# Kernel tuning notes

Hardware: AMD Instinct MI355X
Metric: run time of the kernel (lower is better)

## Reference

```python
import jax, jax.numpy as jnp
import numpy as np

K = 7          # involution kernel size
P = 3          # padding = (K-1)//2
GC = 16        # group_channels in involution
EPS = 1e-5


def bn(x, g, b):
    # training-mode BatchNorm2d forward: per-channel batch stats over (B,H,W)
    m = jnp.mean(x, axis=(0, 2, 3), keepdims=True)
    v = jnp.var(x, axis=(0, 2, 3), keepdims=True)
    return (x - m) * jax.lax.rsqrt(v + EPS) * g[None, :, None, None] + b[None, :, None, None]


def conv1x1(x, w):
    # x: [B,C,H,W], w: [O,C] -> [B,O,H,W]
    return jnp.einsum('bchw,oc->bohw', x, w)


def unfold7(x):
    # torch F.unfold(kernel=7, pad=3, stride=1) -> [B, C, K*K, H, W] (C slowest, matching torch layout)
    B, C, H, W = x.shape
    xp = jnp.pad(x, ((0, 0), (0, 0), (P, P), (P, P)))
    return jnp.stack([xp[:, :, i:i + H, j:j + W] for i in range(K) for j in range(K)], axis=2)


def involution(x, wr, gr, br, ws):
    # kernel generation: 1x1 reduce -> BN -> ReLU -> 1x1 span to G*K*K per-pixel kernels
    B, C, H, W = x.shape
    G = C // GC
    t = jax.nn.relu(bn(conv1x1(x, wr), gr, br))          # [B, C//4, H, W]
    w = conv1x1(t, ws).reshape(B, G, 1, K * K, H, W)     # per-pixel kernels
    p = unfold7(x).reshape(B, G, GC, K * K, H, W)        # unfolded patches
    return jnp.sum(w * p, axis=3).reshape(B, C, H, W)    # multiply-accumulate over K*K


def setup_inputs() -> dict:
    key = jax.random.key(0)
    ks = jax.random.split(key, 14)
    Cin, Cout, mid = 256, 256, 64
    red = mid // 4                 # reduction_ratio = 4
    G = mid // GC                  # groups = 4
    s = lambda *sh: 1.0 / np.sqrt(np.prod(sh[1:]) if len(sh) > 1 else sh[0])
    return {
        'x':  jax.random.normal(ks[0], (8, Cin, 56, 56), jnp.float32),
        'w1': jax.random.normal(ks[1], (mid, Cin), jnp.float32) * s(mid, Cin),
        'g1': jnp.ones((mid,), jnp.float32),
        'b1': jnp.zeros((mid,), jnp.float32),
        'wr': jax.random.normal(ks[2], (red, mid), jnp.float32) * s(red, mid),
        'gr': jnp.ones((red,), jnp.float32),
        'br': jnp.zeros((red,), jnp.float32),
        'ws': jax.random.normal(ks[3], (K * K * G, red), jnp.float32) * s(K * K * G, red),
        'g2': jnp.ones((mid,), jnp.float32),
        'b2': jnp.zeros((mid,), jnp.float32),
        'w3': jax.random.normal(ks[4], (Cout, mid), jnp.float32) * s(Cout, mid),
        'g3': jnp.ones((Cout,), jnp.float32),
        'b3': jnp.zeros((Cout,), jnp.float32),
    }


def reference(x, w1, g1, b1, wr, gr, br, ws, g2, b2, w3, g3, b3):
    out = jax.nn.relu(bn(conv1x1(x, w1), g1, b1))        # conv1 1x1 + BN + ReLU
    out = jax.nn.relu(bn(involution(out, wr, gr, br, ws), g2, b2))  # involution + BN + ReLU
    out = bn(conv1x1(out, w3), g3, b3)                   # conv3 1x1 + BN
    return jax.nn.relu(out + x)                          # residual add + ReLU
```

## Files before the change

kernel.cpp:

```cpp
#include <hip/hip_runtime.h>

#define HW 3136
#define NPIX 25088
#define NBLK 392

#define OFF_Y1   0u
#define OFF_TR   1605632u
#define OFF_WT   2007040u
#define OFF_OUT2 6924288u
#define OFF_Y3   8529920u
#define OFF_ST   14952448u
#define ACC1 0
#define ACCR 128
#define ACC2 160
#define ACC3 288
#define FIN1 800
#define FINR 928
#define FIN2 960
#define FIN3 1088

__device__ __forceinline__ float wave_sum(float v) {
    #pragma unroll
    for (int off = 32; off > 0; off >>= 1) v += __shfl_xor(v, off, 64);
    return v;
}

__device__ __forceinline__ void gl_lds16(const float* g, float* l) {
    __builtin_amdgcn_global_load_lds(
        (const __attribute__((address_space(1))) unsigned int*)g,
        (__attribute__((address_space(3))) unsigned int*)l, 16, 0, 0);
}

__global__ __launch_bounds__(256) void k_wt(const float* __restrict__ w1,
        const float* __restrict__ w3, float* __restrict__ w1t, float* __restrict__ w3t) {
    int i = blockIdx.x * 256 + threadIdx.x;
    if (i < 16384) {
        int oc = i >> 8, ic = i & 255;
        w1t[ic * 64 + oc] = w1[i];
    } else {
        int j = i - 16384;
        int oc = j >> 6, ic = j & 63;
        w3t[ic * 256 + oc] = w3[j];
    }
}

__global__ __launch_bounds__(256) void k_conv1(const float* __restrict__ x,
        const float* __restrict__ w1t, float* __restrict__ y1, float* __restrict__ st) {
    __shared__ float xs[2][64][64];
    __shared__ float ws[2][64][64];
    int t = threadIdx.x, pb = blockIdx.x;
    int b = pb / 49, hw0 = (pb % 49) * 64;
    int tx = t & 15, ty = t >> 4;
    int wv = t >> 6, ln = t & 63;

    #define STAGE(cc, buf)                                                        \
        _Pragma("unroll")                                                         \
        for (int i = 0; i < 4; i++) {                                             \
            int s = i * 4 + wv;                                                   \
            const float* gx = x + (size_t)((b * 256) + (cc) * 64 + s * 4 + (ln >> 4)) * HW \
                              + hw0 + (ln & 15) * 4;                              \
            gl_lds16(gx, &xs[buf][s * 4][0]);                                     \
            const float* gw = w1t + ((cc) * 64 + s * 4) * 64 + ln * 4;            \
            gl_lds16(gw, &ws[buf][s * 4][0]);                                     \
        }

    STAGE(0, 0);
    __syncthreads();
    float acc[4][4];
    #pragma unroll
    for (int i = 0; i < 4; i++)
        #pragma unroll
        for (int j = 0; j < 4; j++) acc[i][j] = 0.f;
    #pragma unroll 1
    for (int cc = 0; cc < 4; cc++) {
        int cur = cc & 1;
        if (cc < 3) STAGE(cc + 1, cur ^ 1);
        #pragma unroll 8
        for (int c = 0; c < 64; c++) {
            float4 xv = *(const float4*)&xs[cur][c][tx * 4];
            float4 wv4 = *(const float4*)&ws[cur][c][ty * 4];
            float xa[4] = {xv.x, xv.y, xv.z, xv.w};
            float wa[4] = {wv4.x, wv4.y, wv4.z, wv4.w};
            #pragma unroll
            for (int i = 0; i < 4; i++)
                #pragma unroll
                for (int j = 0; j < 4; j++) acc[i][j] = fmaf(wa[i], xa[j], acc[i][j]);
        }
        __syncthreads();
    }
    #undef STAGE
    #pragma unroll
    for (int i = 0; i < 4; i++) {
        int oc = ty * 4 + i;
        float4 o = make_float4(acc[i][0], acc[i][1], acc[i][2], acc[i][3]);
        *(float4*)&y1[((b * 64) + oc) * HW + hw0 + tx * 4] = o;
        float s = o.x + o.y + o.z + o.w;
        float q = o.x * o.x + o.y * o.y + o.z * o.z + o.w * o.w;
        #pragma unroll
        for (int off = 1; off <= 8; off <<= 1) {
            s += __shfl_xor(s, off, 64);
            q += __shfl_xor(q, off, 64);
        }
        if (tx == 0) {
            atomicAdd(&st[ACC1 + oc], s);
            atomicAdd(&st[ACC1 + 64 + oc], q);
        }
    }
}

__global__ void k_fin(const float* __restrict__ acc, float* __restrict__ fin,
                      const float* __restrict__ gamma, const float* __restrict__ beta, int C) {
    int c = threadIdx.x;
    if (c < C) {
        float mean = acc[c] * (1.0f / (float)NPIX);
        float var  = acc[C + c] * (1.0f / (float)NPIX) - mean * mean;
        float rstd = rsqrtf(var + 1e-5f);
        float a = gamma[c] * rstd;
        fin[c] = a;
        fin[C + c] = beta[c] - mean * a;
    }
}

__global__ __launch_bounds__(256, 4) void k_bn1_convr(const float* __restrict__ y1,
        const float* __restrict__ wr, float* __restrict__ tr, float* __restrict__ st) {
    __shared__ float ys[64][64];
    __shared__ float wsh[16][64];
    int t = threadIdx.x, pb = blockIdx.x;
    int b = pb / 49, hw0 = (pb % 49) * 64;
    int tx = t & 15, ty = t >> 4;
    #pragma unroll
    for (int i = 0; i < 16; i++) {
        int e = i * 256 + t, c = e >> 6, p = e & 63;
        float v = y1[((b * 64) + c) * HW + hw0 + p];
        ys[c][p] = fmaxf(st[FIN1 + c] * v + st[FIN1 + 64 + c], 0.f);
    }
    #pragma unroll
    for (int i = 0; i < 4; i++) {
        int e = i * 256 + t;
        wsh[e >> 6][e & 63] = wr[e];
    }
    __syncthreads();
    float a0 = 0.f, a1 = 0.f, a2 = 0.f, a3 = 0.f;
    #pragma unroll 8
    for (int c = 0; c < 64; c++) {
        float4 yv = *(const float4*)&ys[c][tx * 4];
        float wv = wsh[ty][c];
        a0 = fmaf(wv, yv.x, a0); a1 = fmaf(wv, yv.y, a1);
        a2 = fmaf(wv, yv.z, a2); a3 = fmaf(wv, yv.w, a3);
    }
    *(float4*)&tr[((b * 16) + ty) * HW + hw0 + tx * 4] = make_float4(a0, a1, a2, a3);
    float s = a0 + a1 + a2 + a3;
    float q = a0 * a0 + a1 * a1 + a2 * a2 + a3 * a3;
    #pragma unroll
    for (int off = 1; off <= 8; off <<= 1) {
        s += __shfl_xor(s, off, 64);
        q += __shfl_xor(q, off, 64);
    }
    if (tx == 0) {
        atomicAdd(&st[ACCR + ty], s);
        atomicAdd(&st[ACCR + 16 + ty], q);
    }
}

__global__ __launch_bounds__(256) void k_invol(const float* __restrict__ y1,
        const float* __restrict__ tr, const float* __restrict__ wsp,
        float* __restrict__ out2, float* __restrict__ st) {
    __shared__ float ts[16][256];
    __shared__ float sw[49][16];
    __shared__ float ps[8][10][64];
    __shared__ float red[4][16];
    int t = threadIdx.x, bidx = blockIdx.x;
    int h = bidx & 1, r2 = bidx >> 1;
    int ht = r2 % 14;
    int bg = r2 / 14;
    int g = bg & 3, b = bg >> 2;
    int h0 = ht * 4;
    int c0 = h * 8;
    #pragma unroll
    for (int i = 0; i < 16; i++) {
        int e = i * 256 + t, c = e >> 8, p = e & 255;
        if (p < 224) {
            float v = tr[((b * 16) + c) * HW + h0 * 56 + p];
            ts[c][p] = fmaxf(st[FINR + c] * v + st[FINR + 16 + c], 0.f);
        }
    }
    for (int e = t; e < 784; e += 256) sw[e >> 4][e & 15] = wsp[g * 784 + e];
    for (int i = 0; i < 20; i++) {
        int e = i * 256 + t;
        int c = e / 640, rem = e - c * 640;
        int r = rem >> 6, wc = rem & 63;
        int gh = h0 + r - 3, gw = wc - 3;
        float v = 0.f;
        if (gh >= 0 && gh < 56 && gw >= 0 && gw < 56) {
            int ch = g * 16 + c0 + c;
            float raw = y1[((b * 64) + ch) * HW + gh * 56 + gw];
            v = fmaxf(st[FIN1 + ch] * raw + st[FIN1 + 64 + ch], 0.f);
        }
        ps[c][r][wc] = v;
    }
    __syncthreads();
    float accv[8];
    #pragma unroll
    for (int c = 0; c < 8; c++) accv[c] = 0.f;
    bool active = t < 224;
    if (active) {
        int lh = t / 56, lw = t % 56;
        float tsr[16];
        #pragma unroll
        for (int c = 0; c < 16; c++) tsr[c] = ts[c][t];
        float kr[49];
        #pragma unroll
        for (int k = 0; k < 49; k++) {
            const float4* swr = (const float4*)&sw[k][0];
            float4 u0 = swr[0], u1 = swr[1], u2 = swr[2], u3 = swr[3];
            float v = u0.x * tsr[0];
            v = fmaf(u0.y, tsr[1], v);  v = fmaf(u0.z, tsr[2], v);  v = fmaf(u0.w, tsr[3], v);
            v = fmaf(u1.x, tsr[4], v);  v = fmaf(u1.y, tsr[5], v);  v = fmaf(u1.z, tsr[6], v);
            v = fmaf(u1.w, tsr[7], v);  v = fmaf(u2.x, tsr[8], v);  v = fmaf(u2.y, tsr[9], v);
            v = fmaf(u2.z, tsr[10], v); v = fmaf(u2.w, tsr[11], v); v = fmaf(u3.x, tsr[12], v);
            v = fmaf(u3.y, tsr[13], v); v = fmaf(u3.z, tsr[14], v); v = fmaf(u3.w, tsr[15], v);
            kr[k] = v;
        }
        #pragma unroll
        for (int k = 0; k < 49; k++) {
            int ki = k / 7, kj = k % 7;
            float kv = kr[k];
            #pragma unroll
            for (int c = 0; c < 8; c++)
                accv[c] = fmaf(kv, ps[c][lh + ki][lw + kj], accv[c]);
        }
        int hw = h0 * 56 + t;
        #pragma unroll
        for (int c = 0; c < 8; c++)
            out2[((b * 64) + g * 16 + c0 + c) * HW + hw] = accv[c];
    }
    int wave = t >> 6, lane = t & 63;
    #pragma unroll
    for (int c = 0; c < 8; c++) {
        float v = active ? accv[c] : 0.f;
        float s  = wave_sum(v);
        float s2 = wave_sum(v * v);
        if (lane == 0) { red[wave][c] = s; red[wave][8 + c] = s2; }
    }
    __syncthreads();
    if (t < 16) {
        float s = red[0][t] + red[1][t] + red[2][t] + red[3][t];
        int c = t & 7, isq = t >> 3;
        atomicAdd(&st[ACC2 + isq * 64 + g * 16 + c0 + c], s);
    }
}

__global__ __launch_bounds__(256, 4) void k_bn2_conv3(const float* __restrict__ out2,
        const float* __restrict__ w3t, float* __restrict__ y3, float* __restrict__ st) {
    __shared__ float os[64][64];
    __shared__ float wst[64][64];
    int t = threadIdx.x, blk = blockIdx.x;
    int occ = blk & 3, pb = blk >> 2;
    int b = pb / 49, hw0 = (pb % 49) * 64;
    int tx = t & 15, ty = t >> 4;
    #pragma unroll
    for (int i = 0; i < 16; i++) {
        int e = i * 256 + t, c = e >> 6, p = e & 63;
        float v = out2[((b * 64) + c) * HW + hw0 + p];
        os[c][p] = fmaxf(st[FIN2 + c] * v + st[FIN2 + 64 + c], 0.f);
        wst[c][p] = w3t[c * 256 + occ * 64 + p];
    }
    __syncthreads();
    float acc[4][4];
    #pragma unroll
    for (int i = 0; i < 4; i++)
        #pragma unroll
        for (int j = 0; j < 4; j++) acc[i][j] = 0.f;
    #pragma unroll 8
    for (int c = 0; c < 64; c++) {
        float4 xv = *(const float4*)&os[c][tx * 4];
        float4 wv = *(const float4*)&wst[c][ty * 4];
        float xa[4] = {xv.x, xv.y, xv.z, xv.w};
        float wa[4] = {wv.x, wv.y, wv.z, wv.w};
        #pragma unroll
        for (int i = 0; i < 4; i++)
            #pragma unroll
            for (int j = 0; j < 4; j++) acc[i][j] = fmaf(wa[i], xa[j], acc[i][j]);
    }
    #pragma unroll
    for (int i = 0; i < 4; i++) {
        int oc = occ * 64 + ty * 4 + i;
        float4 o = make_float4(acc[i][0], acc[i][1], acc[i][2], acc[i][3]);
        *(float4*)&y3[((b * 256) + oc) * HW + hw0 + tx * 4] = o;
        float s = o.x + o.y + o.z + o.w;
        float q = o.x * o.x + o.y * o.y + o.z * o.z + o.w * o.w;
        #pragma unroll
        for (int off = 1; off <= 8; off <<= 1) {
            s += __shfl_xor(s, off, 64);
            q += __shfl_xor(q, off, 64);
        }
        if (tx == 0) {
            atomicAdd(&st[ACC3 + oc], s);
            atomicAdd(&st[ACC3 + 256 + oc], q);
        }
    }
}

__global__ __launch_bounds__(256) void k_final(const float* __restrict__ y3,
        const float* __restrict__ x, float* __restrict__ out, const float* __restrict__ st) {
    int idx = blockIdx.x * 256 + threadIdx.x;
    if (idx < 1605632) {
        int c = (idx / 784) & 255;
        float a = st[FIN3 + c], bb = st[FIN3 + 256 + c];
        float4 v  = ((const float4*)y3)[idx];
        float4 xv = ((const float4*)x)[idx];
        float4 o;
        o.x = fmaxf(a * v.x + bb + xv.x, 0.f);
        o.y = fmaxf(a * v.y + bb + xv.y, 0.f);
        o.z = fmaxf(a * v.z + bb + xv.z, 0.f);
        o.w = fmaxf(a * v.w + bb + xv.w, 0.f);
        ((float4*)out)[idx] = o;
    }
}

extern "C" void kernel_launch(void* const* d_in, const int* in_sizes, int n_in,
                              void* d_out, int out_size, void* d_ws, size_t ws_size,
                              hipStream_t stream) {
    const float* x   = (const float*)d_in[0];
    const float* w1  = (const float*)d_in[1];
    const float* g1  = (const float*)d_in[2];
    const float* b1  = (const float*)d_in[3];
    const float* wr  = (const float*)d_in[4];
    const float* gr  = (const float*)d_in[5];
    const float* br  = (const float*)d_in[6];
    const float* wsp = (const float*)d_in[7];
    const float* g2  = (const float*)d_in[8];
    const float* b2  = (const float*)d_in[9];
    const float* w3  = (const float*)d_in[10];
    const float* g3  = (const float*)d_in[11];
    const float* b3  = (const float*)d_in[12];
    float* out = (float*)d_out;
    float* w   = (float*)d_ws;
    float* y1   = w + OFF_Y1;
    float* tr   = w + OFF_TR;
    float* w1t  = w + OFF_WT;
    float* w3t  = w + OFF_WT + 16384;
    float* out2 = w + OFF_OUT2;
    float* y3   = w + OFF_Y3;
    float* st   = w + OFF_ST;

    hipMemsetAsync(st, 0, 2048 * sizeof(float), stream);
    k_wt<<<128, 256, 0, stream>>>(w1, w3, w1t, w3t);
    k_conv1<<<NBLK, 256, 0, stream>>>(x, w1t, y1, st);
    k_fin<<<1, 64, 0, stream>>>(st + ACC1, st + FIN1, g1, b1, 64);
    k_bn1_convr<<<NBLK, 256, 0, stream>>>(y1, wr, tr, st);
    k_fin<<<1, 64, 0, stream>>>(st + ACCR, st + FINR, gr, br, 16);
    k_invol<<<896, 256, 0, stream>>>(y1, tr, wsp, out2, st);
    k_fin<<<1, 64, 0, stream>>>(st + ACC2, st + FIN2, g2, b2, 64);
    k_bn2_conv3<<<NBLK * 4, 256, 0, stream>>>(out2, w3t, y3, st);
    k_fin<<<1, 256, 0, stream>>>(st + ACC3, st + FIN3, g3, b3, 256);
    k_final<<<6272, 256, 0, stream>>>(y3, x, out, st);
}
```

Baseline: 275.1 us.

## Use bf16 MFMA for conv1 and conv3 with pixel-major transposed bf16 inputs

Replaces the fp32 FMA tiled GEMMs for conv1 and conv3 with bf16 MFMA 16x16x32 instructions. A new pass transposes x into a pixel-major bf16 layout with an XOR-swizzled LDS-friendly addressing. The involution kernel now writes its output as pixel-major bf16, and conv3 runs one block per pixel tile covering all 256 output channels instead of four blocks. The aim is to cut ALU time and memory traffic, at the cost of an extra transpose pass over x and reduced precision from bf16 rounding of activations and weights.

Result: no change. 274.5 us (-0.2%).

```diff
diff --git a/kernel.cpp b/kernel.cpp
--- a/kernel.cpp
+++ b/kernel.cpp
@@ -4,12 +4,17 @@
 #define NPIX 25088
 #define NBLK 392
 
-#define OFF_Y1   0u
-#define OFF_TR   1605632u
-#define OFF_WT   2007040u
-#define OFF_OUT2 6924288u
-#define OFF_Y3   8529920u
-#define OFF_ST   14952448u
+typedef float f32x4 __attribute__((ext_vector_type(4)));
+typedef short short8 __attribute__((ext_vector_type(8)));
+
+#define OFF_Y1    0u
+#define OFF_TR    1605632u
+#define OFF_W1BF  2007040u
+#define OFF_W3BF  2015232u
+#define OFF_XT    2023424u
+#define OFF_OUT2T 5234688u
+#define OFF_Y3    6037504u
+#define OFF_ST    12460032u
 #define ACC1 0
 #define ACCR 128
 #define ACC2 160
@@ -24,84 +29,105 @@
     for (int off = 32; off > 0; off >>= 1) v += __shfl_xor(v, off, 64);
     return v;
 }
-
-__device__ __forceinline__ void gl_lds16(const float* g, float* l) {
+__device__ __forceinline__ unsigned short f2bf(float f) {
+    unsigned u = __float_as_uint(f);
+    u += 0x7FFFu + ((u >> 16) & 1u);
+    return (unsigned short)(u >> 16);
+}
+__device__ __forceinline__ float bf2f(unsigned h) {
+    return __uint_as_float(h << 16);
+}
+__device__ __forceinline__ void gl_lds16(const void* g, void* l) {
     __builtin_amdgcn_global_load_lds(
         (const __attribute__((address_space(1))) unsigned int*)g,
         (__attribute__((address_space(3))) unsigned int*)l, 16, 0, 0);
 }
 
-__global__ __launch_bounds__(256) void k_wt(const float* __restrict__ w1,
-        const float* __restrict__ w3, float* __restrict__ w1t, float* __restrict__ w3t) {
+__global__ __launch_bounds__(256) void k_prep(const float* __restrict__ w1,
+        const float* __restrict__ w3, unsigned short* __restrict__ w1bf,
+        unsigned short* __restrict__ w3bf) {
     int i = blockIdx.x * 256 + threadIdx.x;
-    if (i < 16384) {
-        int oc = i >> 8, ic = i & 255;
-        w1t[ic * 64 + oc] = w1[i];
-    } else {
-        int j = i - 16384;
-        int oc = j >> 6, ic = j & 63;
-        w3t[ic * 256 + oc] = w3[j];
-    }
-}
-
-__global__ __launch_bounds__(256) void k_conv1(const float* __restrict__ x,
-        const float* __restrict__ w1t, float* __restrict__ y1, float* __restrict__ st) {
-    __shared__ float xs[2][64][64];
-    __shared__ float ws[2][64][64];
+    if (i < 16384) w1bf[i] = f2bf(w1[i]);
+    else w3bf[i - 16384] = f2bf(w3[i - 16384]);
+}
+
+__global__ __launch_bounds__(256) void k_tx(const float* __restrict__ x,
+        unsigned short* __restrict__ xt) {
+    __shared__ float lt[64][65];
+    int t = threadIdx.x, bidx = blockIdx.x;
+    int ict = bidx & 3, r = bidx >> 2;
+    int pt = r % 49, b = r / 49;
+    int pix0 = pt * 64, ic0 = ict * 64;
+    #pragma unroll
+    for (int i = 0; i < 16; i++) {
+        int e = i * 256 + t, ic = e >> 6, p = e & 63;
+        lt[ic][p] = x[(size_t)((b * 256) + ic0 + ic) * HW + pix0 + p];
+    }
+    __syncthreads();
+    char* tb = (char*)xt + (size_t)(b * HW + pix0) * 512;
+    #pragma unroll
+    for (int i = 0; i < 2; i++) {
+        int c = i * 256 + t;
+        int p = c >> 3, q = c & 7;
+        uint4 o;
+        o.x = f2bf(lt[q * 8 + 0][p]) | ((unsigned)f2bf(lt[q * 8 + 1][p]) << 16);
+        o.y = f2bf(lt[q * 8 + 2][p]) | ((unsigned)f2bf(lt[q * 8 + 3][p]) << 16);
+        o.z = f2bf(lt[q * 8 + 4][p]) | ((unsigned)f2bf(lt[q * 8 + 5][p]) << 16);
+        o.w = f2bf(lt[q * 8 + 6][p]) | ((unsigned)f2bf(lt[q * 8 + 7][p]) << 16);
+        unsigned d = (unsigned)(p * 512 + (ic0 + q * 8) * 2) ^ (unsigned)((p & 7) << 4);
+        *(uint4*)(tb + d) = o;
+    }
+}
+
+__global__ __launch_bounds__(256, 4) void k_conv1(const unsigned short* __restrict__ xt,
+        const unsigned short* __restrict__ w1bf, float* __restrict__ y1,
+        float* __restrict__ st) {
+    __shared__ unsigned short xs[64 * 256];
     int t = threadIdx.x, pb = blockIdx.x;
     int b = pb / 49, hw0 = (pb % 49) * 64;
-    int tx = t & 15, ty = t >> 4;
-    int wv = t >> 6, ln = t & 63;
-
-    #define STAGE(cc, buf)                                                        \
-        _Pragma("unroll")                                                         \
-        for (int i = 0; i < 4; i++) {                                             \
-            int s = i * 4 + wv;                                                   \
-            const float* gx = x + (size_t)((b * 256) + (cc) * 64 + s * 4 + (ln >> 4)) * HW \
-                              + hw0 + (ln & 15) * 4;                              \
-            gl_lds16(gx, &xs[buf][s * 4][0]);                                     \
-            const float* gw = w1t + ((cc) * 64 + s * 4) * 64 + ln * 4;            \
-            gl_lds16(gw, &ws[buf][s * 4][0]);                                     \
-        }
-
-    STAGE(0, 0);
-    __syncthreads();
-    float acc[4][4];
-    #pragma unroll
-    for (int i = 0; i < 4; i++)
-        #pragma unroll
-        for (int j = 0; j < 4; j++) acc[i][j] = 0.f;
-    #pragma unroll 1
-    for (int cc = 0; cc < 4; cc++) {
-        int cur = cc & 1;
-        if (cc < 3) STAGE(cc + 1, cur ^ 1);
-        #pragma unroll 8
-        for (int c = 0; c < 64; c++) {
-            float4 xv = *(const float4*)&xs[cur][c][tx * 4];
-            float4 wv4 = *(const float4*)&ws[cur][c][ty * 4];
-            float xa[4] = {xv.x, xv.y, xv.z, xv.w};
-            float wa[4] = {wv4.x, wv4.y, wv4.z, wv4.w};
-            #pragma unroll
-            for (int i = 0; i < 4; i++)
-                #pragma unroll
-                for (int j = 0; j < 4; j++) acc[i][j] = fmaf(wa[i], xa[j], acc[i][j]);
-        }
-        __syncthreads();
-    }
-    #undef STAGE
-    #pragma unroll
-    for (int i = 0; i < 4; i++) {
-        int oc = ty * 4 + i;
-        float4 o = make_float4(acc[i][0], acc[i][1], acc[i][2], acc[i][3]);
-        *(float4*)&y1[((b * 64) + oc) * HW + hw0 + tx * 4] = o;
-        float s = o.x + o.y + o.z + o.w;
-        float q = o.x * o.x + o.y * o.y + o.z * o.z + o.w * o.w;
+    int lane = t & 63, wv = t >> 6;
+    int grp = lane >> 4, li = lane & 15;
+    int oc0 = wv * 16;
+    short8 a[8];
+    #pragma unroll
+    for (int s = 0; s < 8; s++)
+        a[s] = *(const short8*)(w1bf + (size_t)(oc0 + li) * 256 + s * 32 + grp * 8);
+    const char* src = (const char*)xt + (size_t)(b * HW + hw0) * 512;
+    char* dst = (char*)xs;
+    #pragma unroll
+    for (int i = 0; i < 8; i++)
+        gl_lds16(src + wv * 8192 + i * 1024 + lane * 16, dst + wv * 8192 + i * 1024);
+    __syncthreads();
+    f32x4 acc[4];
+    #pragma unroll
+    for (int n = 0; n < 4; n++) acc[n] = (f32x4){0.f, 0.f, 0.f, 0.f};
+    #pragma unroll
+    for (int s = 0; s < 8; s++) {
+        #pragma unroll
+        for (int n = 0; n < 4; n++) {
+            int row = n * 16 + li;
+            unsigned o = (unsigned)(row * 512 + s * 64 + grp * 16) ^ (unsigned)((row & 7) << 4);
+            short8 bf = *(const short8*)(dst + o);
+            acc[n] = __builtin_amdgcn_mfma_f32_16x16x32_bf16(a[s], bf, acc[n], 0, 0, 0);
+        }
+    }
+    #pragma unroll
+    for (int n = 0; n < 4; n++)
+        #pragma unroll
+        for (int r = 0; r < 4; r++)
+            y1[(size_t)(b * 64 + oc0 + grp * 4 + r) * HW + hw0 + n * 16 + li] = acc[n][r];
+    #pragma unroll
+    for (int r = 0; r < 4; r++) {
+        float s = acc[0][r] + acc[1][r] + acc[2][r] + acc[3][r];
+        float q = acc[0][r] * acc[0][r] + acc[1][r] * acc[1][r]
+                + acc[2][r] * acc[2][r] + acc[3][r] * acc[3][r];
         #pragma unroll
         for (int off = 1; off <= 8; off <<= 1) {
             s += __shfl_xor(s, off, 64);
             q += __shfl_xor(q, off, 64);
         }
-        if (tx == 0) {
+        if (li == 0) {
+            int oc = oc0 + grp * 4 + r;
             atomicAdd(&st[ACC1 + oc], s);
             atomicAdd(&st[ACC1 + 64 + oc], q);
         }
@@ -164,18 +190,18 @@
 
 __global__ __launch_bounds__(256) void k_invol(const float* __restrict__ y1,
         const float* __restrict__ tr, const float* __restrict__ wsp,
-        float* __restrict__ out2, float* __restrict__ st) {
+        unsigned short* __restrict__ out2t, float* __restrict__ st) {
     __shared__ float ts[16][256];
     __shared__ float sw[49][16];
     __shared__ float ps[8][10][64];
     __shared__ float red[4][16];
     int t = threadIdx.x, bidx = blockIdx.x;
-    int h = bidx & 1, r2 = bidx >> 1;
+    int hh = bidx & 1, r2 = bidx >> 1;
     int ht = r2 % 14;
     int bg = r2 / 14;
     int g = bg & 3, b = bg >> 2;
     int h0 = ht * 4;
-    int c0 = h * 8;
+    int c0 = hh * 8;
     #pragma unroll
     for (int i = 0; i < 16; i++) {
         int e = i * 256 + t, c = e >> 8, p = e & 255;
@@ -230,9 +256,12 @@
                 accv[c] = fmaf(kv, ps[c][lh + ki][lw + kj], accv[c]);
         }
         int hw = h0 * 56 + t;
-        #pragma unroll
-        for (int c = 0; c < 8; c++)
-            out2[((b * 64) + g * 16 + c0 + c) * HW + hw] = accv[c];
+        uint4 o;
+        o.x = f2bf(accv[0]) | ((unsigned)f2bf(accv[1]) << 16);
+        o.y = f2bf(accv[2]) | ((unsigned)f2bf(accv[3]) << 16);
+        o.z = f2bf(accv[4]) | ((unsigned)f2bf(accv[5]) << 16);
+        o.w = f2bf(accv[6]) | ((unsigned)f2bf(accv[7]) << 16);
+        *(uint4*)((char*)out2t + (size_t)(b * HW + hw) * 128 + (g * 16 + c0) * 2) = o;
     }
     int wave = t >> 6, lane = t & 63;
     #pragma unroll
@@ -250,53 +279,89 @@
     }
 }
 
-__global__ __launch_bounds__(256, 4) void k_bn2_conv3(const float* __restrict__ out2,
-        const float* __restrict__ w3t, float* __restrict__ y3, float* __restrict__ st) {
-    __shared__ float os[64][64];
-    __shared__ float wst[64][64];
-    int t = threadIdx.x, blk = blockIdx.x;
-    int occ = blk & 3, pb = blk >> 2;
+__global__ __launch_bounds__(256, 2) void k_bn2c3(const unsigned short* __restrict__ out2t,
+        const unsigned short* __restrict__ w3bf, float* __restrict__ y3,
+        float* __restrict__ st) {
+    __shared__ unsigned short bs[64 * 64];
+    __shared__ float sa[64], sb[64];
+    int t = threadIdx.x, pb = blockIdx.x;
     int b = pb / 49, hw0 = (pb % 49) * 64;
-    int tx = t & 15, ty = t >> 4;
-    #pragma unroll
-    for (int i = 0; i < 16; i++) {
-        int e = i * 256 + t, c = e >> 6, p = e & 63;
-        float v = out2[((b * 64) + c) * HW + hw0 + p];
-        os[c][p] = fmaxf(st[FIN2 + c] * v + st[FIN2 + 64 + c], 0.f);
-        wst[c][p] = w3t[c * 256 + occ * 64 + p];
-    }
-    __syncthreads();
-    float acc[4][4];
-    #pragma unroll
-    for (int i = 0; i < 4; i++)
-        #pragma unroll
-        for (int j = 0; j < 4; j++) acc[i][j] = 0.f;
-    #pragma unroll 8
-    for (int c = 0; c < 64; c++) {
-        float4 xv = *(const float4*)&os[c][tx * 4];
-        float4 wv = *(const float4*)&wst[c][ty * 4];
-        float xa[4] = {xv.x, xv.y, xv.z, xv.w};
-        float wa[4] = {wv.x, wv.y, wv.z, wv.w};
-        #pragma unroll
-        for (int i = 0; i < 4; i++)
+    int lane = t & 63, wv = t >> 6;
+    int grp = lane >> 4, li = lane & 15;
+    if (t < 64) sa[t] = st[FIN2 + t];
+    else if (t < 128) { int c = t - 64; sb[c] = st[FIN2 + 64 + c]; }
+    short8 a[8];
+    #pragma unroll
+    for (int m = 0; m < 4; m++)
+        #pragma unroll
+        for (int s = 0; s < 2; s++)
+            a[m * 2 + s] = *(const short8*)(w3bf
+                + (size_t)(wv * 64 + m * 16 + li) * 64 + s * 32 + grp * 8);
+    __syncthreads();
+    #pragma unroll
+    for (int i = 0; i < 2; i++) {
+        int c = i * 256 + t, p = c >> 3, q = c & 7;
+        uint4 v = *(const uint4*)((const char*)out2t + (size_t)(b * HW + hw0 + p) * 128 + q * 16);
+        float4 fa0 = *(const float4*)&sa[q * 8];
+        float4 fa1 = *(const float4*)&sa[q * 8 + 4];
+        float4 fb0 = *(const float4*)&sb[q * 8];
+        float4 fb1 = *(const float4*)&sb[q * 8 + 4];
+        float e0 = fmaxf(fa0.x * bf2f(v.x & 0xFFFFu) + fb0.x, 0.f);
+        float e1 = fmaxf(fa0.y * bf2f(v.x >> 16) + fb0.y, 0.f);
+        float e2 = fmaxf(fa0.z * bf2f(v.y & 0xFFFFu) + fb0.z, 0.f);
+        float e3 = fmaxf(fa0.w * bf2f(v.y >> 16) + fb0.w, 0.f);
+        float e4 = fmaxf(fa1.x * bf2f(v.z & 0xFFFFu) + fb1.x, 0.f);
+        float e5 = fmaxf(fa1.y * bf2f(v.z >> 16) + fb1.y, 0.f);
+        float e6 = fmaxf(fa1.z * bf2f(v.w & 0xFFFFu) + fb1.z, 0.f);
+        float e7 = fmaxf(fa1.w * bf2f(v.w >> 16) + fb1.w, 0.f);
+        uint4 o;
+        o.x = f2bf(e0) | ((unsigned)f2bf(e1) << 16);
+        o.y = f2bf(e2) | ((unsigned)f2bf(e3) << 16);
+        o.z = f2bf(e4) | ((unsigned)f2bf(e5) << 16);
+        o.w = f2bf(e6) | ((unsigned)f2bf(e7) << 16);
+        unsigned d = (unsigned)(p * 128 + q * 16) ^ (unsigned)((p & 7) << 4);
+        *(uint4*)((char*)bs + d) = o;
+    }
+    __syncthreads();
+    f32x4 acc[4][4];
+    #pragma unroll
+    for (int m = 0; m < 4; m++)
+        #pragma unroll
+        for (int n = 0; n < 4; n++) acc[m][n] = (f32x4){0.f, 0.f, 0.f, 0.f};
+    #pragma unroll
+    for (int s = 0; s < 2; s++)
+        #pragma unroll
+        for (int n = 0; n < 4; n++) {
+            int row = n * 16 + li;
+            unsigned o = (unsigned)(row * 128 + s * 64 + grp * 16) ^ (unsigned)((row & 7) << 4);
+            short8 bf = *(const short8*)((const char*)bs + o);
             #pragma unroll
-            for (int j = 0; j < 4; j++) acc[i][j] = fmaf(wa[i], xa[j], acc[i][j]);
-    }
-    #pragma unroll
-    for (int i = 0; i < 4; i++) {
-        int oc = occ * 64 + ty * 4 + i;
-        float4 o = make_float4(acc[i][0], acc[i][1], acc[i][2], acc[i][3]);
-        *(float4*)&y3[((b * 256) + oc) * HW + hw0 + tx * 4] = o;
-        float s = o.x + o.y + o.z + o.w;
-        float q = o.x * o.x + o.y * o.y + o.z * o.z + o.w * o.w;
-        #pragma unroll
-        for (int off = 1; off <= 8; off <<= 1) {
-            s += __shfl_xor(s, off, 64);
-            q += __shfl_xor(q, off, 64);
-        }
-        if (tx == 0) {
-            atomicAdd(&st[ACC3 + oc], s);
-            atomicAdd(&st[ACC3 + 256 + oc], q);
+            for (int m = 0; m < 4; m++)
+                acc[m][n] = __builtin_amdgcn_mfma_f32_16x16x32_bf16(a[m * 2 + s], bf, acc[m][n], 0, 0, 0);
+        }
+    #pragma unroll
+    for (int m = 0; m < 4; m++) {
+        #pragma unroll
+        for (int n = 0; n < 4; n++)
+            #pragma unroll
+            for (int r = 0; r < 4; r++)
+                y3[(size_t)(b * 256 + wv * 64 + m * 16 + grp * 4 + r) * HW
+                   + hw0 + n * 16 + li] = acc[m][n][r];
+        #pragma unroll
+        for (int r = 0; r < 4; r++) {
+            float s = acc[m][0][r] + acc[m][1][r] + acc[m][2][r] + acc[m][3][r];
+            float q = acc[m][0][r] * acc[m][0][r] + acc[m][1][r] * acc[m][1][r]
+                    + acc[m][2][r] * acc[m][2][r] + acc[m][3][r] * acc[m][3][r];
+            #pragma unroll
+            for (int off = 1; off <= 8; off <<= 1) {
+                s += __shfl_xor(s, off, 64);
+                q += __shfl_xor(q, off, 64);
+            }
+            if (li == 0) {
+                int oc = wv * 64 + m * 16 + grp * 4 + r;
+                atomicAdd(&st[ACC3 + oc], s);
+                atomicAdd(&st[ACC3 + 256 + oc], q);
+            }
         }
     }
 }
@@ -336,23 +401,25 @@
     const float* b3  = (const float*)d_in[12];
     float* out = (float*)d_out;
     float* w   = (float*)d_ws;
-    float* y1   = w + OFF_Y1;
-    float* tr   = w + OFF_TR;
-    float* w1t  = w + OFF_WT;
-    float* w3t  = w + OFF_WT + 16384;
-    float* out2 = w + OFF_OUT2;
-    float* y3   = w + OFF_Y3;
-    float* st   = w + OFF_ST;
+    float* y1    = w + OFF_Y1;
+    float* tr    = w + OFF_TR;
+    unsigned short* w1bf  = (unsigned short*)(w + OFF_W1BF);
+    unsigned short* w3bf  = (unsigned short*)(w + OFF_W3BF);
+    unsigned short* xt    = (unsigned short*)(w + OFF_XT);
+    unsigned short* out2t = (unsigned short*)(w + OFF_OUT2T);
+    float* y3    = w + OFF_Y3;
+    float* st    = w + OFF_ST;
 
     hipMemsetAsync(st, 0, 2048 * sizeof(float), stream);
-    k_wt<<<128, 256, 0, stream>>>(w1, w3, w1t, w3t);
-    k_conv1<<<NBLK, 256, 0, stream>>>(x, w1t, y1, st);
+    k_prep<<<128, 256, 0, stream>>>(w1, w3, w1bf, w3bf);
+    k_tx<<<1568, 256, 0, stream>>>(x, xt);
+    k_conv1<<<NBLK, 256, 0, stream>>>(xt, w1bf, y1, st);
     k_fin<<<1, 64, 0, stream>>>(st + ACC1, st + FIN1, g1, b1, 64);
     k_bn1_convr<<<NBLK, 256, 0, stream>>>(y1, wr, tr, st);
     k_fin<<<1, 64, 0, stream>>>(st + ACCR, st + FINR, gr, br, 16);
-    k_invol<<<896, 256, 0, stream>>>(y1, tr, wsp, out2, st);
+    k_invol<<<896, 256, 0, stream>>>(y1, tr, wsp, out2t, st);
     k_fin<<<1, 64, 0, stream>>>(st + ACC2, st + FIN2, g2, b2, 64);
-    k_bn2_conv3<<<NBLK * 4, 256, 0, stream>>>(out2, w3t, y3, st);
+    k_bn2c3<<<NBLK, 256, 0, stream>>>(out2t, w3bf, y3, st);
     k_fin<<<1, 256, 0, stream>>>(st + ACC3, st + FIN3, g3, b3, 256);
     k_final<<<6272, 256, 0, stream>>>(y3, x, out, st);
 }
```
